# Performance work log

Hardware: AMD Instinct MI355X
Metric: run time of the kernel (lower is better)

## Reference

```python
import jax, jax.numpy as jnp
import numpy as np

HEAD_DIM = 256
ROPE_THETA = 1000000.0
EPS = 1e-6


def rmsnorm(x, w):
    # torch.nn.RMSNorm: x / sqrt(mean(x^2) + eps) * w, over last dim
    var = jnp.mean(jnp.square(x), axis=-1, keepdims=True)
    return x * jax.lax.rsqrt(var + EPS) * w


def apply_rope(x):
    # x: [b, h, L, head_dim]; rotate-half-split RoPE as in the source
    L, hd = x.shape[-2], x.shape[-1]
    half = hd // 2
    pos = jnp.arange(L, dtype=x.dtype)
    idx = jnp.arange(half, dtype=x.dtype)
    inv_freq = 1.0 / (ROPE_THETA ** (2.0 * idx / hd))
    freqs = pos[:, None] * inv_freq[None, :]          # [L, half]
    cos = jnp.cos(freqs)[None, None]                  # [1,1,L,half]
    sin = jnp.sin(freqs)[None, None]
    x1, x2 = x[..., :half], x[..., half:]
    return jnp.concatenate([x1 * cos - x2 * sin, x1 * sin + x2 * cos], axis=-1)


def setup_inputs() -> dict:
    key = jax.random.key(0)
    ks = jax.random.split(key, 7)
    B, L, D = 2, 2048, 2048
    H, HD = 8, HEAD_DIM
    s = lambda fan_in: 1.0 / np.sqrt(fan_in)
    return {
        "x": jax.random.normal(ks[0], (B, L, D), jnp.float32),
        "q_proj": jax.random.normal(ks[1], (H * HD, D), jnp.float32) * s(D),
        "k_proj": jax.random.normal(ks[2], (HD, D), jnp.float32) * s(D),
        "v_proj": jax.random.normal(ks[3], (HD, D), jnp.float32) * s(D),
        "o_proj": jax.random.normal(ks[4], (D, H * HD), jnp.float32) * s(H * HD),
        "q_norm": jnp.ones((HD,), jnp.float32),
        "k_norm": jnp.ones((HD,), jnp.float32),
    }


def reference(x, q_proj, k_proj, v_proj, o_proj, q_norm, k_norm):
    B, L, D = x.shape
    HD = k_proj.shape[0]
    H = q_proj.shape[0] // HD

    # projections (Linear weight is [out, in])
    k = rmsnorm(x @ k_proj.T, k_norm)                 # [B, L, HD]
    q = rmsnorm((x @ q_proj.T).reshape(B, L, H, HD), q_norm)
    v = x @ v_proj.T                                  # [B, L, HD]

    q = q.transpose(0, 2, 1, 3)                       # [B, H, L, HD]
    k = k[:, None]                                    # [B, 1, L, HD] (MQA)
    v = v[:, None]

    q = apply_rope(q)
    k = apply_rope(k)

    scores = jnp.matmul(q, jnp.swapaxes(k, -1, -2)) / jnp.sqrt(
        jnp.asarray(256.0, x.dtype))                  # [B, H, L, L]
    causal = jnp.tril(jnp.ones((L, L), bool))
    scores = jnp.where(causal, scores, -jnp.inf)
    w = jax.nn.softmax(scores, axis=-1)
    ctx = jnp.matmul(w, v)                            # [B, H, L, HD]
    ctx = ctx.transpose(0, 2, 1, 3).reshape(B, L, H * HD)
    return ctx @ o_proj.T
```

## Files before the change

### kernel.cpp

```cpp
#include <hip/hip_runtime.h>
#include <hip/hip_bf16.h>
#include <stdint.h>

typedef __bf16 bf16;
typedef bf16 bf16x8 __attribute__((ext_vector_type(8)));
typedef float f32x4 __attribute__((ext_vector_type(4)));

__device__ __forceinline__ bf16x8 load8(const float* p) {
    const f32x4 lo = *(const f32x4*)p;
    const f32x4 hi = *(const f32x4*)(p + 4);
    bf16x8 v;
#pragma unroll
    for (int r = 0; r < 4; ++r) { v[r] = (bf16)lo[r]; v[4 + r] = (bf16)hi[r]; }
    return v;
}
__device__ __forceinline__ bf16x8 load8(const bf16* p) {
    return *(const bf16x8*)p;
}

__device__ __forceinline__ void gload16(const bf16* g, bf16* l) {
    __builtin_amdgcn_global_load_lds((const __attribute__((address_space(1))) void*)g,
                                     (__attribute__((address_space(3))) void*)l, 16, 0, 0);
}

__global__ __launch_bounds__(256) void cvt_bf16(const float* __restrict__ src,
                                                bf16* __restrict__ dst, int n8) {
    int idx = blockIdx.x * 256 + threadIdx.x;
    const int stride = gridDim.x * 256;
    for (; idx < n8; idx += stride) {
        const f32x4 lo = *(const f32x4*)(src + (size_t)idx * 8);
        const f32x4 hi = *(const f32x4*)(src + (size_t)idx * 8 + 4);
        bf16x8 v;
#pragma unroll
        for (int r = 0; r < 4; ++r) { v[r] = (bf16)lo[r]; v[4 + r] = (bf16)hi[r]; }
        *(bf16x8*)(dst + (size_t)idx * 8) = v;
    }
}

__global__ __launch_bounds__(256) void cvt_qkvx(const float* __restrict__ x,
                                                const float* __restrict__ q,
                                                const float* __restrict__ k,
                                                const float* __restrict__ v,
                                                bf16* __restrict__ dst,
                                                int nx8, int nq8, int nk8, int nv8) {
    const int total = nx8 + nq8 + nk8 + nv8;
    int idx = blockIdx.x * 256 + threadIdx.x;
    const int stride = gridDim.x * 256;
    for (; idx < total; idx += stride) {
        const float* s;
        int off;
        if (idx < nx8)                   { s = x; off = idx; }
        else if (idx < nx8 + nq8)        { s = q; off = idx - nx8; }
        else if (idx < nx8 + nq8 + nk8)  { s = k; off = idx - nx8 - nq8; }
        else                             { s = v; off = idx - nx8 - nq8 - nk8; }
        const f32x4 lo = *(const f32x4*)(s + (size_t)off * 8);
        const f32x4 hi = *(const f32x4*)(s + (size_t)off * 8 + 4);
        bf16x8 o;
#pragma unroll
        for (int r = 0; r < 4; ++r) { o[r] = (bf16)lo[r]; o[4 + r] = (bf16)hi[r]; }
        *(bf16x8*)(dst + (size_t)idx * 8) = o;
    }
}

template <typename AT, typename BT, typename CT>
__global__ __launch_bounds__(256) void gemm_bt(const AT* __restrict__ A,
                                               const BT* __restrict__ B,
                                               CT* __restrict__ C,
                                               int M, int N, int K) {
    __shared__ __align__(16) bf16 As[128 * 32];
    __shared__ __align__(16) bf16 Bs[128 * 32];
    const int tid  = threadIdx.x;
    const int wave = tid >> 6, lane = tid & 63;
    const int quad = lane >> 4, l16 = lane & 15;
    const int m0 = blockIdx.y * 128, n0 = blockIdx.x * 128;
    const int wr = (wave >> 1) * 64, wc = (wave & 1) * 64;

    const int srow = wave * 32 + (lane >> 2);
    const int scol = (lane & 3) * 8;
    const AT* Ag = A + (size_t)(m0 + srow) * K + scol;
    const BT* Bg = B + (size_t)(n0 + srow) * K + scol;
    bf16* Asw = &As[srow * 32 + scol];
    bf16* Bsw = &Bs[srow * 32 + scol];

    f32x4 acc[4][4] = {};

    for (int k0 = 0; k0 < K; k0 += 32) {
        const bf16x8 av0 = load8(Ag + k0);
        const bf16x8 av1 = load8(Ag + k0 + (size_t)16 * K);
        const bf16x8 bv0 = load8(Bg + k0);
        const bf16x8 bv1 = load8(Bg + k0 + (size_t)16 * K);
        __syncthreads();
        *(bf16x8*)(Asw)           = av0;
        *(bf16x8*)(Asw + 16 * 32) = av1;
        *(bf16x8*)(Bsw)           = bv0;
        *(bf16x8*)(Bsw + 16 * 32) = bv1;
        __syncthreads();

        bf16x8 a[4], b[4];
#pragma unroll
        for (int i = 0; i < 4; ++i)
            a[i] = *(const bf16x8*)&As[(wr + i * 16 + l16) * 32 + quad * 8];
#pragma unroll
        for (int j = 0; j < 4; ++j)
            b[j] = *(const bf16x8*)&Bs[(wc + j * 16 + l16) * 32 + quad * 8];
#pragma unroll
        for (int i = 0; i < 4; ++i)
#pragma unroll
            for (int j = 0; j < 4; ++j)
                acc[i][j] = __builtin_amdgcn_mfma_f32_16x16x32_bf16(a[i], b[j], acc[i][j], 0, 0, 0);
    }

#pragma unroll
    for (int i = 0; i < 4; ++i)
#pragma unroll
        for (int j = 0; j < 4; ++j) {
            const int row = m0 + wr + i * 16 + quad * 4;
            const int col = n0 + wc + j * 16 + l16;
#pragma unroll
            for (int r = 0; r < 4; ++r)
                C[(size_t)(row + r) * N + col] = (CT)acc[i][j][r];
        }
}

template <typename CT>
__global__ __launch_bounds__(256) void gemm_bb(const bf16* __restrict__ A,
                                               const bf16* __restrict__ B,
                                               CT* __restrict__ C,
                                               int M, int N, int K) {
    __shared__ __align__(16) bf16 As[128 * 32];
    __shared__ __align__(16) bf16 Bs[128 * 32];
    const int tid  = threadIdx.x;
    const int wave = tid >> 6, lane = tid & 63;
    const int quad = lane >> 4, l16 = lane & 15;
    const int m0 = blockIdx.y * 128, n0 = blockIdx.x * 128;
    const int wr = (wave >> 1) * 64, wc = (wave & 1) * 64;

    const int srow = tid >> 2, scol = (tid & 3) * 8;
    const bf16* Ag = A + (size_t)(m0 + srow) * K + scol;
    const bf16* Bg = B + (size_t)(n0 + srow) * K + scol;
    bf16* Adst = As + wave * 512;
    bf16* Bdst = Bs + wave * 512;

    f32x4 acc[4][4] = {};

    for (int k0 = 0; k0 < K; k0 += 32) {
        __syncthreads();
        gload16(Ag + k0, Adst);
        gload16(Ag + k0 + (size_t)64 * K, Adst + 2048);
        gload16(Bg + k0, Bdst);
        gload16(Bg + k0 + (size_t)64 * K, Bdst + 2048);
        __syncthreads();

        bf16x8 a[4], b[4];
#pragma unroll
        for (int i = 0; i < 4; ++i)
            a[i] = *(const bf16x8*)&As[(wr + i * 16 + l16) * 32 + quad * 8];
#pragma unroll
        for (int j = 0; j < 4; ++j)
            b[j] = *(const bf16x8*)&Bs[(wc + j * 16 + l16) * 32 + quad * 8];
#pragma unroll
        for (int i = 0; i < 4; ++i)
#pragma unroll
            for (int j = 0; j < 4; ++j)
                acc[i][j] = __builtin_amdgcn_mfma_f32_16x16x32_bf16(a[i], b[j], acc[i][j], 0, 0, 0);
    }

#pragma unroll
    for (int i = 0; i < 4; ++i)
#pragma unroll
        for (int j = 0; j < 4; ++j) {
            const int row = m0 + wr + i * 16 + quad * 4;
            const int col = n0 + wc + j * 16 + l16;
#pragma unroll
            for (int r = 0; r < 4; ++r)
                C[(size_t)(row + r) * N + col] = (CT)acc[i][j][r];
        }
}

__global__ __launch_bounds__(256) void gemm_qkv(const bf16* __restrict__ A,
                                                const bf16* __restrict__ W,
                                                bf16* __restrict__ Cq,
                                                bf16* __restrict__ Ck,
                                                bf16* __restrict__ Cv,
                                                int M, int K) {
    __shared__ __align__(16) bf16 As[128 * 32];
    __shared__ __align__(16) bf16 Bs[128 * 32];
    const int tid  = threadIdx.x;
    const int wave = tid >> 6, lane = tid & 63;
    const int quad = lane >> 4, l16 = lane & 15;
    const int m0 = blockIdx.y * 128, n0 = blockIdx.x * 128;
    const int wr = (wave >> 1) * 64, wc = (wave & 1) * 64;

    const int srow = tid >> 2, scol = (tid & 3) * 8;
    const bf16* Ag = A + (size_t)(m0 + srow) * K + scol;
    const bf16* Bg = W + (size_t)(n0 + srow) * K + scol;
    bf16* Adst = As + wave * 512;
    bf16* Bdst = Bs + wave * 512;

    f32x4 acc[4][4] = {};

    for (int k0 = 0; k0 < K; k0 += 32) {
        __syncthreads();
        gload16(Ag + k0, Adst);
        gload16(Ag + k0 + (size_t)64 * K, Adst + 2048);
        gload16(Bg + k0, Bdst);
        gload16(Bg + k0 + (size_t)64 * K, Bdst + 2048);
        __syncthreads();

        bf16x8 a[4], b[4];
#pragma unroll
        for (int i = 0; i < 4; ++i)
            a[i] = *(const bf16x8*)&As[(wr + i * 16 + l16) * 32 + quad * 8];
#pragma unroll
        for (int j = 0; j < 4; ++j)
            b[j] = *(const bf16x8*)&Bs[(wc + j * 16 + l16) * 32 + quad * 8];
#pragma unroll
        for (int i = 0; i < 4; ++i)
#pragma unroll
            for (int j = 0; j < 4; ++j)
                acc[i][j] = __builtin_amdgcn_mfma_f32_16x16x32_bf16(a[i], b[j], acc[i][j], 0, 0, 0);
    }

    bf16* cb; int cw, coff;
    if (n0 < 2048)      { cb = Cq; cw = 2048; coff = 0; }
    else if (n0 < 2304) { cb = Ck; cw = 256;  coff = 2048; }
    else                { cb = Cv; cw = 256;  coff = 2304; }

#pragma unroll
    for (int i = 0; i < 4; ++i)
#pragma unroll
        for (int j = 0; j < 4; ++j) {
            const int row = m0 + wr + i * 16 + quad * 4;
            const int col = n0 + wc + j * 16 + l16 - coff;
#pragma unroll
            for (int r = 0; r < 4; ++r)
                cb[(size_t)(row + r) * cw + col] = (bf16)acc[i][j][r];
        }
}

__device__ __forceinline__ void norm_rope_body(bf16* __restrict__ x,
                                               const float* __restrict__ w,
                                               int rid, int L, int div, int t) {
    const size_t base = (size_t)rid * 256;
    const float v = (float)x[base + t];
    float ss = v * v;
#pragma unroll
    for (int off = 32; off >= 1; off >>= 1) ss += __shfl_xor(ss, off);

    __shared__ float wsum[4];
    __shared__ float buf[256];
    const int wave = t >> 6, lane = t & 63;
    if (lane == 0) wsum[wave] = ss;
    __syncthreads();
    const float var = (wsum[0] + wsum[1] + wsum[2] + wsum[3]) * (1.0f / 256.0f);
    const float inv = rsqrtf(var + 1e-6f);
    buf[t] = v * inv * w[t];
    __syncthreads();

    const int pos = (rid / div) % L;
    const int i = t & 127;
    const float freq = (float)pos * exp2f(-(float)i * (19.93156857f / 128.0f));
    const float c = cosf(freq), s = sinf(freq);
    const float x1 = buf[i], x2 = buf[i + 128];
    const float out = (t < 128) ? (x1 * c - x2 * s) : (x1 * s + x2 * c);
    x[base + t] = (bf16)out;
}

__global__ __launch_bounds__(256) void norm_rope(bf16* __restrict__ x,
                                                 const float* __restrict__ w,
                                                 int L, int div) {
    norm_rope_body(x, w, blockIdx.x, L, div, threadIdx.x);
}

__global__ __launch_bounds__(256) void norm_rope2(bf16* __restrict__ Q,
                                                  bf16* __restrict__ K,
                                                  const float* __restrict__ qw,
                                                  const float* __restrict__ kw,
                                                  int L, int MH) {
    const int row = blockIdx.x;
    if (row < MH) norm_rope_body(Q, qw, row, L, 8, threadIdx.x);
    else          norm_rope_body(K, kw, row - MH, L, 1, threadIdx.x);
}

__global__ __launch_bounds__(256) void transpose_v(const bf16* __restrict__ V,
                                                   bf16* __restrict__ Vt, int L) {
    __shared__ bf16 tile[32][33];
    const int b = blockIdx.z;
    const int l0 = blockIdx.x * 32, d0 = blockIdx.y * 32;
    const int tx = threadIdx.x & 31, ty = threadIdx.x >> 5;
#pragma unroll
    for (int i = 0; i < 32; i += 8)
        tile[ty + i][tx] = V[((size_t)b * L + l0 + ty + i) * 256 + d0 + tx];
    __syncthreads();
#pragma unroll
    for (int i = 0; i < 32; i += 8)
        Vt[((size_t)b * 256 + d0 + ty + i) * L + l0 + tx] = tile[tx][ty + i];
}

__device__ __forceinline__ int kswz(int r, int c) { return r * 256 + (c ^ ((r & 7) << 3)); }
__device__ __forceinline__ int vswz(int r, int c) { return r * 64  + (c ^ ((r & 7) << 3)); }

template <int SPLIT>
__global__ __launch_bounds__(256, 2) void flash_attn(const bf16* __restrict__ Q,
                                                     const bf16* __restrict__ K,
                                                     const bf16* __restrict__ Vt,
                                                     bf16* __restrict__ Ctx,
                                                     float* __restrict__ P0,
                                                     float* __restrict__ P1,
                                                     float* __restrict__ ML0,
                                                     float* __restrict__ ML1, int L) {
    constexpr int H = 8, HD = 256;
    extern __shared__ __align__(16) bf16 smem[];
    bf16* Ks = smem;
    bf16* Vs = Ks + 64 * 256;
    bf16* Ps = Vs + 256 * 64;

    const int z = blockIdx.x, h = blockIdx.y;
    const int b    = SPLIT ? ((int)blockIdx.z >> 1) : (int)blockIdx.z;
    const int half = SPLIT ? ((int)blockIdx.z & 1) : 0;
    const int tid = threadIdx.x;
    const int wave = tid >> 6, lane = tid & 63;
    const int quad = lane >> 4, l16 = lane & 15;
    const int nqt = L / 64;

    const bf16* Kb = K + (size_t)b * L * HD;
    const bf16* Vb = Vt + (size_t)b * HD * L;
    bf16* Pw = Ps + wave * 16 * 64;

    const int krow = tid >> 5, kcol = (tid & 31) * 8;
    const int vrow = tid >> 3, vcol = (tid & 7) * 8;
    const int kcs = kcol ^ ((krow & 7) << 3);
    const int vcs = vcol ^ ((vrow & 7) << 3);
    bf16* kdst = Ks + wave * 512;
    bf16* vdst = Vs + wave * 512;

    for (int pass = 0; pass < 2; ++pass) {
        const int qt = pass ? z : (nqt - 1 - z);
        const int q0 = qt * 64 + wave * 16;
        const int s  = qt + 1;
        const int c0 = (s + 1) >> 1;
        const int kt0 = (SPLIT && half) ? c0 : 0;
        const int cnt = SPLIT ? (half ? s - c0 : c0) : s;

        bf16x8 qf[8];
        {
            const bf16* qbase = Q + ((size_t)(b * L + q0 + l16) * H + h) * HD + quad * 8;
#pragma unroll
            for (int kc = 0; kc < 8; ++kc) qf[kc] = *(const bf16x8*)(qbase + kc * 32);
        }

        f32x4 Oacc[16] = {};
        float mrow[4], lrow[4];
#pragma unroll
        for (int r = 0; r < 4; ++r) { mrow[r] = -1e30f; lrow[r] = 0.0f; }

        __syncthreads();
        if (cnt > 0) {
            const int kv0 = kt0 * 64;
#pragma unroll
            for (int i = 0; i < 8; ++i)
                gload16(Kb + (size_t)(kv0 + i * 8 + krow) * HD + kcs, kdst + i * 2048);
#pragma unroll
            for (int i = 0; i < 8; ++i)
                gload16(Vb + (size_t)(i * 32 + vrow) * L + kv0 + vcs, vdst + i * 2048);
        }
        __syncthreads();

        for (int it = 0; it < cnt; ++it) {
            const int kt = kt0 + it;
            const int kv0 = kt * 64;
            const int nv0 = kv0 + 64;
            const bool more = (it + 1 < cnt);

            f32x4 S[4];
#pragma unroll
            for (int nt = 0; nt < 4; ++nt) {
                f32x4 slo = {0.f, 0.f, 0.f, 0.f}, shi = {0.f, 0.f, 0.f, 0.f};
                const int krw = nt * 16 + l16;
#pragma unroll
                for (int kc = 0; kc < 4; ++kc)
                    slo = __builtin_amdgcn_mfma_f32_16x16x32_bf16(qf[kc], *(const bf16x8*)&Ks[kswz(krw, quad * 8 + kc * 32)], slo, 0, 0, 0);
#pragma unroll
                for (int kc = 4; kc < 8; ++kc)
                    shi = __builtin_amdgcn_mfma_f32_16x16x32_bf16(qf[kc], *(const bf16x8*)&Ks[kswz(krw, quad * 8 + kc * 32)], shi, 0, 0, 0);
                S[nt] = slo + shi;
            }

            __syncthreads();
            if (more) {
#pragma unroll
                for (int i = 0; i < 8; ++i)
                    gload16(Kb + (size_t)(nv0 + i * 8 + krow) * HD + kcs, kdst + i * 2048);
            }

            float rowmax[4] = {-1e30f, -1e30f, -1e30f, -1e30f};
            const bool diag = (kt == qt);
#pragma unroll
            for (int nt = 0; nt < 4; ++nt) {
                const int col = kv0 + nt * 16 + l16;
#pragma unroll
                for (int r = 0; r < 4; ++r) {
                    float sv = S[nt][r] * 0.0625f;
                    if (diag && col > q0 + quad * 4 + r) sv = -1e30f;
                    S[nt][r] = sv;
                    rowmax[r] = fmaxf(rowmax[r], sv);
                }
            }
#pragma unroll
            for (int off = 1; off < 16; off <<= 1)
#pragma unroll
                for (int r = 0; r < 4; ++r)
                    rowmax[r] = fmaxf(rowmax[r], __shfl_xor(rowmax[r], off));

            float alpha[4], rsum[4];
#pragma unroll
            for (int r = 0; r < 4; ++r) {
                const float mnew = fmaxf(mrow[r], rowmax[r]);
                alpha[r] = __expf(mrow[r] - mnew);
                mrow[r] = mnew;
                rsum[r] = 0.0f;
            }
#pragma unroll
            for (int nt = 0; nt < 4; ++nt)
#pragma unroll
                for (int r = 0; r < 4; ++r) {
                    const float p = __expf(S[nt][r] - mrow[r]);
                    rsum[r] += p;
                    Pw[vswz(quad * 4 + r, nt * 16 + l16)] = (bf16)p;
                }
#pragma unroll
            for (int off = 1; off < 16; off <<= 1)
#pragma unroll
                for (int r = 0; r < 4; ++r) rsum[r] += __shfl_xor(rsum[r], off);
#pragma unroll
            for (int r = 0; r < 4; ++r) lrow[r] = lrow[r] * alpha[r] + rsum[r];

#pragma unroll
            for (int nt = 0; nt < 16; ++nt)
#pragma unroll
                for (int r = 0; r < 4; ++r) Oacc[nt][r] *= alpha[r];

            bf16x8 pf[2];
#pragma unroll
            for (int ks = 0; ks < 2; ++ks)
                pf[ks] = *(const bf16x8*)&Pw[vswz(l16, ks * 32 + quad * 8)];
#pragma unroll
            for (int nt = 0; nt < 16; ++nt) {
                const int vrw = nt * 16 + l16;
                f32x4 o = Oacc[nt];
#pragma unroll
                for (int ks = 0; ks < 2; ++ks)
                    o = __builtin_amdgcn_mfma_f32_16x16x32_bf16(pf[ks], *(const bf16x8*)&Vs[vswz(vrw, ks * 32 + quad * 8)], o, 0, 0, 0);
                Oacc[nt] = o;
            }

            __syncthreads();
            if (more) {
#pragma unroll
                for (int i = 0; i < 8; ++i)
                    gload16(Vb + (size_t)(i * 32 + vrow) * L + nv0 + vcs, vdst + i * 2048);
            }
        }

        if (SPLIT) {
            float* Pd  = half ? P1 : P0;
            float* MLd = half ? ML1 : ML0;
            const size_t rowbase = (((size_t)b * H + h) * nqt + qt) * 64 + wave * 16;
            float* prow = Pd + rowbase * 256;
#pragma unroll
            for (int nt = 0; nt < 16; ++nt)
#pragma unroll
                for (int r = 0; r < 4; ++r)
                    prow[(size_t)(quad * 4 + r) * 256 + nt * 16 + l16] = Oacc[nt][r];
            if (l16 == 0) {
#pragma unroll
                for (int r = 0; r < 4; ++r) {
                    const size_t rr = rowbase + quad * 4 + r;
                    MLd[rr * 2 + 0] = mrow[r];
                    MLd[rr * 2 + 1] = lrow[r];
                }
            }
        } else {
            bf16* obase = Ctx + ((size_t)(b * L + q0) * H + h) * HD;
#pragma unroll
            for (int nt = 0; nt < 16; ++nt)
#pragma unroll
                for (int r = 0; r < 4; ++r) {
                    const float val = Oacc[nt][r] / lrow[r];
                    obase[(size_t)(quad * 4 + r) * (H * HD) + nt * 16 + l16] = (bf16)val;
                }
        }
    }
}

__global__ __launch_bounds__(256) void merge_partials(const float* __restrict__ P0,
                                                      const float* __restrict__ P1,
                                                      const float* __restrict__ ML0,
                                                      const float* __restrict__ ML1,
                                                      bf16* __restrict__ Ctx, int L) {
    constexpr int H = 8, HD = 256;
    const int qt = blockIdx.x, h = blockIdx.y, b = blockIdx.z;
    const int nqt = L / 64;
    const int t = threadIdx.x;
    const size_t rowbase = (((size_t)b * H + h) * nqt + qt) * 64;
    const int rlo = t >> 6;
    const int d = (t & 63) * 4;
#pragma unroll
    for (int it = 0; it < 16; ++it) {
        const int r = it * 4 + rlo;
        const size_t rr = rowbase + r;
        const float m0 = ML0[rr * 2], l0 = ML0[rr * 2 + 1];
        const float m1 = ML1[rr * 2], l1 = ML1[rr * 2 + 1];
        const float mn = fmaxf(m0, m1);
        const float a0 = __expf(m0 - mn), a1 = __expf(m1 - mn);
        const float linv = 1.0f / (l0 * a0 + l1 * a1);
        const f32x4 o0 = *(const f32x4*)&P0[rr * 256 + d];
        const f32x4 o1 = *(const f32x4*)&P1[rr * 256 + d];
        bf16* op = Ctx + ((size_t)(b * L + qt * 64 + r) * H + h) * HD + d;
#pragma unroll
        for (int j = 0; j < 4; ++j) op[j] = (bf16)((o0[j] * a0 + o1[j] * a1) * linv);
    }
}

extern "C" void kernel_launch(void* const* d_in, const int* in_sizes, int n_in,
                              void* d_out, int out_size, void* d_ws, size_t ws_size,
                              hipStream_t stream) {
    const float* x      = (const float*)d_in[0];
    const float* q_proj = (const float*)d_in[1];
    const float* k_proj = (const float*)d_in[2];
    const float* v_proj = (const float*)d_in[3];
    const float* o_proj = (const float*)d_in[4];
    const float* q_norm = (const float*)d_in[5];
    const float* k_norm = (const float*)d_in[6];
    float* out = (float*)d_out;

    constexpr int B = 2, L = 2048, D = 2048, H = 8, HD = 256;
    constexpr int M = B * L;
    constexpr int NQT = L / 64;
    constexpr int NQKV = D + 2 * HD;
    constexpr int FLASH_LDS = (64 * 256 + 256 * 64 + 4 * 16 * 64) * 2;

    static bool attr_set = false;
    if (!attr_set) {
        (void)hipFuncSetAttribute((const void*)flash_attn<0>,
                                  hipFuncAttributeMaxDynamicSharedMemorySize, FLASH_LDS);
        (void)hipFuncSetAttribute((const void*)flash_attn<1>,
                                  hipFuncAttributeMaxDynamicSharedMemorySize, FLASH_LDS);
        attr_set = true;
    }

    bf16* Qw  = (bf16*)d_ws;
    bf16* Kw  = Qw  + (size_t)M * D;
    bf16* Vw  = Kw  + (size_t)M * HD;
    bf16* Vtw = Vw  + (size_t)M * HD;
    bf16* Ctx = Vtw + (size_t)M * HD;

    char* region = (char*)(Ctx + (size_t)M * D);
    bf16* Xb   = (bf16*)region;
    bf16* Wqkv = Xb + (size_t)M * D;
    constexpr size_t PELEMS  = (size_t)B * H * NQT * 64 * 256;
    constexpr size_t MLELEMS = (size_t)B * H * NQT * 64 * 2;
    float* P0  = (float*)region;
    float* P1  = P0 + PELEMS;
    float* ML0 = P1 + PELEMS;
    float* ML1 = ML0 + MLELEMS;
    bf16*  Ob  = (bf16*)region;
    const size_t ws_needed = (size_t)((char*)(ML1 + MLELEMS) - (char*)d_ws);

    if (ws_size >= ws_needed) {
        cvt_qkvx<<<2048, 256, 0, stream>>>(x, q_proj, k_proj, v_proj, Xb,
                                           M * D / 8, D * D / 8, HD * D / 8, HD * D / 8);
        gemm_qkv<<<dim3(NQKV / 128, M / 128), 256, 0, stream>>>(Xb, Wqkv, Qw, Kw, Vw, M, D);
        norm_rope2<<<M * H + M, 256, 0, stream>>>(Qw, Kw, q_norm, k_norm, L, M * H);
        transpose_v<<<dim3(L / 32, HD / 32, B), 256, 0, stream>>>(Vw, Vtw, L);
        flash_attn<1><<<dim3(L / 128, H, B * 2), 256, FLASH_LDS, stream>>>(Qw, Kw, Vtw, Ctx,
                                                                           P0, P1, ML0, ML1, L);
        merge_partials<<<dim3(NQT, H, B), 256, 0, stream>>>(P0, P1, ML0, ML1, Ctx, L);
        cvt_bf16<<<2048, 256, 0, stream>>>(o_proj, Ob, D * D / 8);
        gemm_bb<float><<<dim3(D / 128, M / 128), 256, 0, stream>>>(Ctx, Ob, out, M, D, D);
    } else {
        gemm_bt<float, float, bf16><<<dim3(D / 128, M / 128), 256, 0, stream>>>(x, q_proj, Qw, M, D, D);
        gemm_bt<float, float, bf16><<<dim3(HD / 128, M / 128), 256, 0, stream>>>(x, k_proj, Kw, M, HD, D);
        gemm_bt<float, float, bf16><<<dim3(HD / 128, M / 128), 256, 0, stream>>>(x, v_proj, Vw, M, HD, D);
        norm_rope<<<M * H, 256, 0, stream>>>(Qw, q_norm, L, H);
        norm_rope<<<M, 256, 0, stream>>>(Kw, k_norm, L, 1);
        transpose_v<<<dim3(L / 32, HD / 32, B), 256, 0, stream>>>(Vw, Vtw, L);
        flash_attn<0><<<dim3(L / 128, H, B), 256, FLASH_LDS, stream>>>(Qw, Kw, Vtw, Ctx,
                                                                       P0, P1, ML0, ML1, L);
        gemm_bt<bf16, float, float><<<dim3(D / 128, M / 128), 256, 0, stream>>>(Ctx, o_proj, out, M, D, D);
    }
}
```

Baseline: 354.6 us.

## Process 128-row query tiles per block so each K/V tile serves two subtiles

```diff
diff --git a/kernel.cpp b/kernel.cpp
--- a/kernel.cpp
+++ b/kernel.cpp
@@ -301,7 +301,7 @@
 __device__ __forceinline__ int vswz(int r, int c) { return r * 64  + (c ^ ((r & 7) << 3)); }
 
 template <int SPLIT>
-__global__ __launch_bounds__(256, 2) void flash_attn(const bf16* __restrict__ Q,
+__global__ __launch_bounds__(256, 1) void flash_attn(const bf16* __restrict__ Q,
                                                      const bf16* __restrict__ K,
                                                      const bf16* __restrict__ Vt,
                                                      bf16* __restrict__ Ctx,
@@ -321,11 +321,11 @@
     const int tid = threadIdx.x;
     const int wave = tid >> 6, lane = tid & 63;
     const int quad = lane >> 4, l16 = lane & 15;
-    const int nqt = L / 64;
+    const int nQT = L / 128;
 
     const bf16* Kb = K + (size_t)b * L * HD;
     const bf16* Vb = Vt + (size_t)b * HD * L;
-    bf16* Pw = Ps + wave * 16 * 64;
+    bf16* Pw = Ps + wave * 2048;
 
     const int krow = tid >> 5, kcol = (tid & 31) * 8;
     const int vrow = tid >> 3, vcol = (tid & 7) * 8;
@@ -335,27 +335,30 @@
     bf16* vdst = Vs + wave * 512;
 
     for (int pass = 0; pass < 2; ++pass) {
-        const int qt = pass ? z : (nqt - 1 - z);
-        const int q0 = qt * 64 + wave * 16;
-        const int s  = qt + 1;
-        const int c0 = (s + 1) >> 1;
+        const int qt  = pass ? z : (nQT - 1 - z);
+        const int qb0 = qt * 128 + wave * 32;
+        const int s   = 2 * (qt + 1);
+        const int c0  = qt + 1;
         const int kt0 = (SPLIT && half) ? c0 : 0;
-        const int cnt = SPLIT ? (half ? s - c0 : c0) : s;
-
-        bf16x8 qf[8];
+        const int cnt = SPLIT ? c0 : s;
+
+        bf16x8 qf[2][8];
+#pragma unroll
+        for (int sub = 0; sub < 2; ++sub) {
+            const bf16* qbase = Q + ((size_t)(b * L + qb0 + sub * 16 + l16) * H + h) * HD + quad * 8;
+#pragma unroll
+            for (int kc = 0; kc < 8; ++kc) qf[sub][kc] = *(const bf16x8*)(qbase + kc * 32);
+        }
+
+        f32x4 Oacc[2][16] = {};
+        float mrow[2][4], lrow[2][4];
+#pragma unroll
+        for (int sub = 0; sub < 2; ++sub)
+#pragma unroll
+            for (int r = 0; r < 4; ++r) { mrow[sub][r] = -1e30f; lrow[sub][r] = 0.0f; }
+
+        __syncthreads();
         {
-            const bf16* qbase = Q + ((size_t)(b * L + q0 + l16) * H + h) * HD + quad * 8;
-#pragma unroll
-            for (int kc = 0; kc < 8; ++kc) qf[kc] = *(const bf16x8*)(qbase + kc * 32);
-        }
-
-        f32x4 Oacc[16] = {};
-        float mrow[4], lrow[4];
-#pragma unroll
-        for (int r = 0; r < 4; ++r) { mrow[r] = -1e30f; lrow[r] = 0.0f; }
-
-        __syncthreads();
-        if (cnt > 0) {
             const int kv0 = kt0 * 64;
 #pragma unroll
             for (int i = 0; i < 8; ++i)
@@ -372,18 +375,18 @@
             const int nv0 = kv0 + 64;
             const bool more = (it + 1 < cnt);
 
-            f32x4 S[4];
+            f32x4 S[2][4];
 #pragma unroll
             for (int nt = 0; nt < 4; ++nt) {
-                f32x4 slo = {0.f, 0.f, 0.f, 0.f}, shi = {0.f, 0.f, 0.f, 0.f};
+                f32x4 s0 = {0.f, 0.f, 0.f, 0.f}, s1 = {0.f, 0.f, 0.f, 0.f};
                 const int krw = nt * 16 + l16;
 #pragma unroll
-                for (int kc = 0; kc < 4; ++kc)
-                    slo = __builtin_amdgcn_mfma_f32_16x16x32_bf16(qf[kc], *(const bf16x8*)&Ks[kswz(krw, quad * 8 + kc * 32)], slo, 0, 0, 0);
-#pragma unroll
-                for (int kc = 4; kc < 8; ++kc)
-                    shi = __builtin_amdgcn_mfma_f32_16x16x32_bf16(qf[kc], *(const bf16x8*)&Ks[kswz(krw, quad * 8 + kc * 32)], shi, 0, 0, 0);
-                S[nt] = slo + shi;
+                for (int kc = 0; kc < 8; ++kc) {
+                    const bf16x8 kf = *(const bf16x8*)&Ks[kswz(krw, quad * 8 + kc * 32)];
+                    s0 = __builtin_amdgcn_mfma_f32_16x16x32_bf16(qf[0][kc], kf, s0, 0, 0, 0);
+                    s1 = __builtin_amdgcn_mfma_f32_16x16x32_bf16(qf[1][kc], kf, s1, 0, 0, 0);
+                }
+                S[0][nt] = s0; S[1][nt] = s1;
             }
 
             __syncthreads();
@@ -393,65 +396,89 @@
                     gload16(Kb + (size_t)(nv0 + i * 8 + krow) * HD + kcs, kdst + i * 2048);
             }
 
-            float rowmax[4] = {-1e30f, -1e30f, -1e30f, -1e30f};
-            const bool diag = (kt == qt);
-#pragma unroll
-            for (int nt = 0; nt < 4; ++nt) {
-                const int col = kv0 + nt * 16 + l16;
-#pragma unroll
-                for (int r = 0; r < 4; ++r) {
-                    float sv = S[nt][r] * 0.0625f;
-                    if (diag && col > q0 + quad * 4 + r) sv = -1e30f;
-                    S[nt][r] = sv;
-                    rowmax[r] = fmaxf(rowmax[r], sv);
+            float rowmax[2][4];
+#pragma unroll
+            for (int sub = 0; sub < 2; ++sub) {
+                const int q0s = qb0 + sub * 16;
+                const bool dm = (kv0 + 63 > q0s);
+#pragma unroll
+                for (int r = 0; r < 4; ++r) rowmax[sub][r] = -1e30f;
+#pragma unroll
+                for (int nt = 0; nt < 4; ++nt) {
+                    const int col = kv0 + nt * 16 + l16;
+#pragma unroll
+                    for (int r = 0; r < 4; ++r) {
+                        float sv = S[sub][nt][r] * 0.0625f;
+                        if (dm && col > q0s + quad * 4 + r) sv = -1e30f;
+                        S[sub][nt][r] = sv;
+                        rowmax[sub][r] = fmaxf(rowmax[sub][r], sv);
+                    }
                 }
             }
 #pragma unroll
             for (int off = 1; off < 16; off <<= 1)
 #pragma unroll
+                for (int sub = 0; sub < 2; ++sub)
+#pragma unroll
+                    for (int r = 0; r < 4; ++r)
+                        rowmax[sub][r] = fmaxf(rowmax[sub][r], __shfl_xor(rowmax[sub][r], off));
+
+            float alpha[2][4], rsum[2][4];
+#pragma unroll
+            for (int sub = 0; sub < 2; ++sub)
+#pragma unroll
+                for (int r = 0; r < 4; ++r) {
+                    const float mnew = fmaxf(mrow[sub][r], rowmax[sub][r]);
+                    alpha[sub][r] = __expf(mrow[sub][r] - mnew);
+                    mrow[sub][r] = mnew;
+                    rsum[sub][r] = 0.0f;
+                }
+#pragma unroll
+            for (int sub = 0; sub < 2; ++sub)
+#pragma unroll
+                for (int nt = 0; nt < 4; ++nt)
+#pragma unroll
+                    for (int r = 0; r < 4; ++r) {
+                        const float p = __expf(S[sub][nt][r] - mrow[sub][r]);
+                        rsum[sub][r] += p;
+                        Pw[sub * 1024 + vswz(quad * 4 + r, nt * 16 + l16)] = (bf16)p;
+                    }
+#pragma unroll
+            for (int off = 1; off < 16; off <<= 1)
+#pragma unroll
+                for (int sub = 0; sub < 2; ++sub)
+#pragma unroll
+                    for (int r = 0; r < 4; ++r) rsum[sub][r] += __shfl_xor(rsum[sub][r], off);
+#pragma unroll
+            for (int sub = 0; sub < 2; ++sub)
+#pragma unroll
                 for (int r = 0; r < 4; ++r)
-                    rowmax[r] = fmaxf(rowmax[r], __shfl_xor(rowmax[r], off));
-
-            float alpha[4], rsum[4];
-#pragma unroll
-            for (int r = 0; r < 4; ++r) {
-                const float mnew = fmaxf(mrow[r], rowmax[r]);
-                alpha[r] = __expf(mrow[r] - mnew);
-                mrow[r] = mnew;
-                rsum[r] = 0.0f;
-            }
-#pragma unroll
-            for (int nt = 0; nt < 4; ++nt)
-#pragma unroll
-                for (int r = 0; r < 4; ++r) {
-                    const float p = __expf(S[nt][r] - mrow[r]);
-                    rsum[r] += p;
-                    Pw[vswz(quad * 4 + r, nt * 16 + l16)] = (bf16)p;
-                }
-#pragma unroll
-            for (int off = 1; off < 16; off <<= 1)
-#pragma unroll
-                for (int r = 0; r < 4; ++r) rsum[r] += __shfl_xor(rsum[r], off);
-#pragma unroll
-            for (int r = 0; r < 4; ++r) lrow[r] = lrow[r] * alpha[r] + rsum[r];
-
-#pragma unroll
-            for (int nt = 0; nt < 16; ++nt)
-#pragma unroll
-                for (int r = 0; r < 4; ++r) Oacc[nt][r] *= alpha[r];
-
-            bf16x8 pf[2];
-#pragma unroll
-            for (int ks = 0; ks < 2; ++ks)
-                pf[ks] = *(const bf16x8*)&Pw[vswz(l16, ks * 32 + quad * 8)];
+                    lrow[sub][r] = lrow[sub][r] * alpha[sub][r] + rsum[sub][r];
+
+#pragma unroll
+            for (int sub = 0; sub < 2; ++sub)
+#pragma unroll
+                for (int nt = 0; nt < 16; ++nt)
+#pragma unroll
+                    for (int r = 0; r < 4; ++r) Oacc[sub][nt][r] *= alpha[sub][r];
+
+            bf16x8 pf[2][2];
+#pragma unroll
+            for (int sub = 0; sub < 2; ++sub)
+#pragma unroll
+                for (int ks = 0; ks < 2; ++ks)
+                    pf[sub][ks] = *(const bf16x8*)&Pw[sub * 1024 + vswz(l16, ks * 32 + quad * 8)];
 #pragma unroll
             for (int nt = 0; nt < 16; ++nt) {
                 const int vrw = nt * 16 + l16;
-                f32x4 o = Oacc[nt];
-#pragma unroll
-                for (int ks = 0; ks < 2; ++ks)
-                    o = __builtin_amdgcn_mfma_f32_16x16x32_bf16(pf[ks], *(const bf16x8*)&Vs[vswz(vrw, ks * 32 + quad * 8)], o, 0, 0, 0);
-                Oacc[nt] = o;
+                f32x4 o0 = Oacc[0][nt], o1 = Oacc[1][nt];
+#pragma unroll
+                for (int ks = 0; ks < 2; ++ks) {
+                    const bf16x8 vf = *(const bf16x8*)&Vs[vswz(vrw, ks * 32 + quad * 8)];
+                    o0 = __builtin_amdgcn_mfma_f32_16x16x32_bf16(pf[0][ks], vf, o0, 0, 0, 0);
+                    o1 = __builtin_amdgcn_mfma_f32_16x16x32_bf16(pf[1][ks], vf, o1, 0, 0, 0);
+                }
+                Oacc[0][nt] = o0; Oacc[1][nt] = o1;
             }
 
             __syncthreads();
@@ -465,30 +492,36 @@
         if (SPLIT) {
             float* Pd  = half ? P1 : P0;
             float* MLd = half ? ML1 : ML0;
-            const size_t rowbase = (((size_t)b * H + h) * nqt + qt) * 64 + wave * 16;
-            float* prow = Pd + rowbase * 256;
-#pragma unroll
-            for (int nt = 0; nt < 16; ++nt)
-#pragma unroll
-                for (int r = 0; r < 4; ++r)
-                    prow[(size_t)(quad * 4 + r) * 256 + nt * 16 + l16] = Oacc[nt][r];
-            if (l16 == 0) {
-#pragma unroll
-                for (int r = 0; r < 4; ++r) {
-                    const size_t rr = rowbase + quad * 4 + r;
-                    MLd[rr * 2 + 0] = mrow[r];
-                    MLd[rr * 2 + 1] = lrow[r];
+#pragma unroll
+            for (int sub = 0; sub < 2; ++sub) {
+                const size_t rowbase = (size_t)(b * H + h) * L + qb0 + sub * 16;
+                float* prow = Pd + rowbase * 256;
+#pragma unroll
+                for (int nt = 0; nt < 16; ++nt)
+#pragma unroll
+                    for (int r = 0; r < 4; ++r)
+                        prow[(size_t)(quad * 4 + r) * 256 + nt * 16 + l16] = Oacc[sub][nt][r];
+                if (l16 == 0) {
+#pragma unroll
+                    for (int r = 0; r < 4; ++r) {
+                        const size_t rr = rowbase + quad * 4 + r;
+                        MLd[rr * 2 + 0] = mrow[sub][r];
+                        MLd[rr * 2 + 1] = lrow[sub][r];
+                    }
                 }
             }
         } else {
-            bf16* obase = Ctx + ((size_t)(b * L + q0) * H + h) * HD;
-#pragma unroll
-            for (int nt = 0; nt < 16; ++nt)
-#pragma unroll
-                for (int r = 0; r < 4; ++r) {
-                    const float val = Oacc[nt][r] / lrow[r];
-                    obase[(size_t)(quad * 4 + r) * (H * HD) + nt * 16 + l16] = (bf16)val;
-                }
+#pragma unroll
+            for (int sub = 0; sub < 2; ++sub) {
+                bf16* obase = Ctx + ((size_t)(b * L + qb0 + sub * 16) * H + h) * HD;
+#pragma unroll
+                for (int nt = 0; nt < 16; ++nt)
+#pragma unroll
+                    for (int r = 0; r < 4; ++r) {
+                        const float val = Oacc[sub][nt][r] / lrow[sub][r];
+                        obase[(size_t)(quad * 4 + r) * (H * HD) + nt * 16 + l16] = (bf16)val;
+                    }
+            }
         }
     }
 }
@@ -500,9 +533,8 @@
                                                       bf16* __restrict__ Ctx, int L) {
     constexpr int H = 8, HD = 256;
     const int qt = blockIdx.x, h = blockIdx.y, b = blockIdx.z;
-    const int nqt = L / 64;
     const int t = threadIdx.x;
-    const size_t rowbase = (((size_t)b * H + h) * nqt + qt) * 64;
+    const size_t rowbase = (size_t)(b * H + h) * L + qt * 64;
     const int rlo = t >> 6;
     const int d = (t & 63) * 4;
 #pragma unroll
@@ -536,9 +568,8 @@
 
     constexpr int B = 2, L = 2048, D = 2048, H = 8, HD = 256;
     constexpr int M = B * L;
-    constexpr int NQT = L / 64;
     constexpr int NQKV = D + 2 * HD;
-    constexpr int FLASH_LDS = (64 * 256 + 256 * 64 + 4 * 16 * 64) * 2;
+    constexpr int FLASH_LDS = (64 * 256 + 256 * 64 + 4 * 2 * 16 * 64) * 2;
 
     static bool attr_set = false;
     if (!attr_set) {
@@ -558,8 +589,8 @@
     char* region = (char*)(Ctx + (size_t)M * D);
     bf16* Xb   = (bf16*)region;
     bf16* Wqkv = Xb + (size_t)M * D;
-    constexpr size_t PELEMS  = (size_t)B * H * NQT * 64 * 256;
-    constexpr size_t MLELEMS = (size_t)B * H * NQT * 64 * 2;
+    constexpr size_t PELEMS  = (size_t)B * H * L * 256;
+    constexpr size_t MLELEMS = (size_t)B * H * L * 2;
     float* P0  = (float*)region;
     float* P1  = P0 + PELEMS;
     float* ML0 = P1 + PELEMS;
@@ -573,9 +604,9 @@
         gemm_qkv<<<dim3(NQKV / 128, M / 128), 256, 0, stream>>>(Xb, Wqkv, Qw, Kw, Vw, M, D);
         norm_rope2<<<M * H + M, 256, 0, stream>>>(Qw, Kw, q_norm, k_norm, L, M * H);
         transpose_v<<<dim3(L / 32, HD / 32, B), 256, 0, stream>>>(Vw, Vtw, L);
-        flash_attn<1><<<dim3(L / 128, H, B * 2), 256, FLASH_LDS, stream>>>(Qw, Kw, Vtw, Ctx,
+        flash_attn<1><<<dim3(L / 256, H, B * 2), 256, FLASH_LDS, stream>>>(Qw, Kw, Vtw, Ctx,
                                                                            P0, P1, ML0, ML1, L);
-        merge_partials<<<dim3(NQT, H, B), 256, 0, stream>>>(P0, P1, ML0, ML1, Ctx, L);
+        merge_partials<<<dim3(L / 64, H, B), 256, 0, stream>>>(P0, P1, ML0, ML1, Ctx, L);
         cvt_bf16<<<2048, 256, 0, stream>>>(o_proj, Ob, D * D / 8);
         gemm_bb<float><<<dim3(D / 128, M / 128), 256, 0, stream>>>(Ctx, Ob, out, M, D, D);
     } else {
@@ -585,7 +616,7 @@
         norm_rope<<<M * H, 256, 0, stream>>>(Qw, q_norm, L, H);
         norm_rope<<<M, 256, 0, stream>>>(Kw, k_norm, L, 1);
         transpose_v<<<dim3(L / 32, HD / 32, B), 256, 0, stream>>>(Vw, Vtw, L);
-        flash_attn<0><<<dim3(L / 128, H, B), 256, FLASH_LDS, stream>>>(Qw, Kw, Vtw, Ctx,
+        flash_attn<0><<<dim3(L / 256, H, B), 256, FLASH_LDS, stream>>>(Qw, Kw, Vtw, Ctx,
                                                                        P0, P1, ML0, ML1, L);
         gemm_bt<bf16, float, float><<<dim3(D / 128, M / 128), 256, 0, stream>>>(Ctx, o_proj, out, M, D, D);
     }
```

New measurement: 383.2 us. 1.08x slower.
